# Optimization experiments

Measured on AMD Instinct MI355X. Metric: run time of the kernel, lower is better.

The kernel has to match this reference:

```python
import jax, jax.numpy as jnp
import numpy as np

N_NODES = 100000
N_EDGES = 3200000
N_FEAT = 128
EMB = 64


def setup_inputs() -> dict:
    key = jax.random.key(0)
    ks = jax.random.split(key, 10)
    x = jax.random.normal(ks[0], (N_NODES, N_FEAT), dtype=jnp.float32)
    edge_index = jax.random.randint(ks[1], (2, N_EDGES), 0, N_NODES, dtype=jnp.int64)
    batch_index = jnp.zeros((N_NODES,), dtype=jnp.int64)
    def glorot(k, fan_in, fan_out):
        s = jnp.sqrt(2.0 / (fan_in + fan_out)).astype(jnp.float32)
        return jax.random.normal(k, (fan_in, fan_out), dtype=jnp.float32) * s
    return {
        "x": x,
        "edge_index": edge_index,
        "batch_index": batch_index,
        "W0": glorot(ks[2], N_FEAT, EMB), "b0": jnp.zeros((EMB,), jnp.float32),
        "W1": glorot(ks[3], EMB, EMB),    "b1": jnp.zeros((EMB,), jnp.float32),
        "W2": glorot(ks[4], EMB, EMB),    "b2": jnp.zeros((EMB,), jnp.float32),
        "W3": glorot(ks[5], EMB, EMB),    "b3": jnp.zeros((EMB,), jnp.float32),
        "Wout": glorot(ks[6], EMB, 1),    "bout": jnp.zeros((1,), jnp.float32),
    }


def _gcn_norm(edge_index, n_nodes):
    # Add self-loops, compute symmetric normalization D^{-1/2} A_hat D^{-1/2}.
    loops = jnp.arange(n_nodes, dtype=edge_index.dtype)
    src = jnp.concatenate([edge_index[0], loops])  # message sources
    dst = jnp.concatenate([edge_index[1], loops])  # aggregation targets
    ones = jnp.ones(src.shape[0], dtype=jnp.float32)
    deg = jax.ops.segment_sum(ones, dst, num_segments=n_nodes)
    dinv = jnp.where(deg > 0, jax.lax.rsqrt(deg), 0.0)
    norm = dinv[src] * dinv[dst]  # [E + N]
    return src, dst, norm


def _gcn_conv(h, src, dst, norm, W, b, n_nodes):
    h = h @ W                              # [N, out]
    msg = h[src] * norm[:, None]           # gather + scale
    agg = jax.ops.segment_sum(msg, dst, num_segments=n_nodes)  # scatter-add
    return agg + b


def reference(x, edge_index, batch_index, W0, b0, W1, b1, W2, b2, W3, b3, Wout, bout):
    n = x.shape[0]
    src, dst, norm = _gcn_norm(edge_index, n)
    y = _gcn_conv(x, src, dst, norm, W0, b0, n)
    y = _gcn_conv(y, src, dst, norm, W1, b1, n)
    y = _gcn_conv(y, src, dst, norm, W2, b2, n)
    y = _gcn_conv(y, src, dst, norm, W3, b3, n)
    out = y @ Wout + bout
    return (out, y)
```

## Files before the change

kernel.cpp:

```cpp
#include <hip/hip_runtime.h>
#include <hip/hip_fp16.h>


#define FEAT 128
#define EMB 64
#define BINSHIFT 8
#define BINSIZE 256
#define NBIN 391
#define CHUNK 8192


__global__ __launch_bounds__(256) void bin_count_k(
    const int* __restrict__ dst, int* __restrict__ bincnt, int E) {
    __shared__ int hist[NBIN];
    int t = threadIdx.x;
    int base = blockIdx.x * CHUNK;
    int end = min(base + CHUNK, E);
    for (int i = t; i < NBIN; i += 256) hist[i] = 0;
    __syncthreads();
    for (int e = base + t; e < end; e += 256)
        atomicAdd(&hist[dst[e] >> BINSHIFT], 1);
    __syncthreads();
    for (int b = t; b < NBIN; b += 256) {
        int c = hist[b];
        if (c > 0) atomicAdd(&bincnt[b], c);
    }
}

__global__ void binscan_k(const int* __restrict__ bincnt, int* __restrict__ binptr,
                          int* __restrict__ bincur, int nbin, int E) {
    __shared__ int s[512];
    int t = threadIdx.x;
    int v = (t < nbin) ? bincnt[t] : 0;
    s[t] = v;
    __syncthreads();
    for (int off = 1; off < 512; off <<= 1) {
        int tv = (t >= off) ? s[t - off] : 0;
        __syncthreads();
        s[t] += tv;
        __syncthreads();
    }
    if (t < nbin) {
        int excl = s[t] - v;
        binptr[t] = excl;
        bincur[t] = excl;
    }
    if (t == 0) binptr[nbin] = E;
}

__global__ __launch_bounds__(256) void bin_edges_k(
    const int* __restrict__ src, const int* __restrict__ dst,
    int* __restrict__ bincur, int* __restrict__ ebuf, int E) {
    __shared__ int hist[NBIN];
    __shared__ int lcur[NBIN];
    int t = threadIdx.x;
    int base = blockIdx.x * CHUNK;
    int end = min(base + CHUNK, E);
    for (int i = t; i < NBIN; i += 256) hist[i] = 0;
    __syncthreads();
    for (int e = base + t; e < end; e += 256)
        atomicAdd(&hist[dst[e] >> BINSHIFT], 1);
    __syncthreads();
    for (int b = t; b < NBIN; b += 256) {
        int c = hist[b];
        lcur[b] = (c > 0) ? atomicAdd(&bincur[b], c) : 0;
    }
    __syncthreads();
    for (int e = base + t; e < end; e += 256) {
        int d = dst[e];
        int bin = d >> BINSHIFT;
        int r = atomicAdd(&lcur[bin], 1);
        ebuf[r] = src[e] | ((d & (BINSIZE - 1)) << 24);
    }
}

__global__ __launch_bounds__(256) void build_csr_k(
    const int* __restrict__ ebuf, const int* __restrict__ binptr,
    int* __restrict__ rowptr, float* __restrict__ dinv,
    int* __restrict__ col, int N, int E, int nbin) {
    __shared__ int lcnt[BINSIZE];
    __shared__ int lscan[BINSIZE];
    __shared__ int lcur[BINSIZE];
    int b = blockIdx.x;
    int t = threadIdx.x;
    int n0 = b << BINSHIFT;
    int e0 = binptr[b];
    int e1 = binptr[b + 1];

    lcnt[t] = 0;
    __syncthreads();
    for (int i = e0 + t; i < e1; i += 256)
        atomicAdd(&lcnt[((unsigned)ebuf[i]) >> 24], 1);
    __syncthreads();

    int v = lcnt[t];
    lscan[t] = v;
    __syncthreads();
    for (int off = 1; off < 256; off <<= 1) {
        int tv = (t >= off) ? lscan[t - off] : 0;
        __syncthreads();
        lscan[t] += tv;
        __syncthreads();
    }
    int excl = e0 + lscan[t] - v;
    lcur[t] = excl;
    if (n0 + t < N) {
        rowptr[n0 + t] = excl;
        dinv[n0 + t] = 1.0f / sqrtf((float)(v + 1));
    }
    if (b == nbin - 1 && t == 0) rowptr[N] = E;
    __syncthreads();

    for (int i = e0 + t; i < e1; i += 256) {
        int w = ebuf[i];
        int dl = ((unsigned)w) >> 24;
        int p = atomicAdd(&lcur[dl], 1);
        col[p] = (w & 0xFFFFFF) << 7;
    }
}


#define AKP 68

template <int K>
__global__ __launch_bounds__(256) void gemm_scale_k(
    const float* __restrict__ H, const float* __restrict__ W,
    const float* __restrict__ dinv, __half* __restrict__ G, int N) {
    __shared__ float Ws[K * EMB];
    __shared__ float As[64 * AKP];
    int t = threadIdx.x;
    int r0blk = blockIdx.x * 64;

    for (int i = t * 4; i < K * EMB; i += 1024)
        *(float4*)(Ws + i) = *(const float4*)(W + i);

    int tc = t & 15;
    int tr = t >> 4;
    int j0 = tc * 4;
    int r0 = r0blk + tr * 4;

    float acc[4][4] = {{0.f}};

    for (int k0 = 0; k0 < K; k0 += 64) {
#pragma unroll
        for (int n = 0; n < 4; n++) {
            int idx = t + n * 256;
            int row = idx >> 4;
            int cg  = idx & 15;
            int r = r0blk + row;
            if (r >= N) r = N - 1;
            *(float4*)(As + row * AKP + cg * 4) =
                *(const float4*)(H + (size_t)r * K + k0 + cg * 4);
        }
        __syncthreads();

#pragma unroll 2
        for (int k = 0; k < 64; k += 4) {
            float4 a[4];
#pragma unroll
            for (int i = 0; i < 4; i++)
                a[i] = *(const float4*)(As + (tr * 4 + i) * AKP + k);
#pragma unroll
            for (int kk = 0; kk < 4; kk++) {
                float4 wv = *(const float4*)(Ws + (k0 + k + kk) * EMB + j0);
#pragma unroll
                for (int i = 0; i < 4; i++) {
                    float av = (kk == 0) ? a[i].x : (kk == 1) ? a[i].y
                             : (kk == 2) ? a[i].z : a[i].w;
                    acc[i][0] = fmaf(av, wv.x, acc[i][0]);
                    acc[i][1] = fmaf(av, wv.y, acc[i][1]);
                    acc[i][2] = fmaf(av, wv.z, acc[i][2]);
                    acc[i][3] = fmaf(av, wv.w, acc[i][3]);
                }
            }
        }
        __syncthreads();
    }

#pragma unroll
    for (int i = 0; i < 4; i++) {
        if (r0 + i < N) {
            float s = dinv[r0 + i];
            union { __half2 h2[2]; float2 f2; } o;
            o.h2[0] = __floats2half2_rn(acc[i][0] * s, acc[i][1] * s);
            o.h2[1] = __floats2half2_rn(acc[i][2] * s, acc[i][3] * s);
            *(float2*)(G + (size_t)(r0 + i) * EMB + j0) = o.f2;
        }
    }
}


__device__ __forceinline__ void h8_acc(float (&a)[8], float4 raw) {
    union { float4 f4; __half2 h2[4]; } u;
    u.f4 = raw;
    float2 p0 = __half22float2(u.h2[0]);
    float2 p1 = __half22float2(u.h2[1]);
    float2 p2 = __half22float2(u.h2[2]);
    float2 p3 = __half22float2(u.h2[3]);
    a[0] += p0.x; a[1] += p0.y; a[2] += p1.x; a[3] += p1.y;
    a[4] += p2.x; a[5] += p2.y; a[6] += p3.x; a[7] += p3.y;
}

__device__ __forceinline__ void agg_node8(const __half* __restrict__ G,
                                          const int* __restrict__ coff,
                                          int s, int e, int selfoff,
                                          int grp, int f8, float (&r)[8]) {
    const char* Gb = (const char*)G + f8 * 16;
    float a0[8] = {0.f, 0.f, 0.f, 0.f, 0.f, 0.f, 0.f, 0.f};
    float a1[8] = {0.f, 0.f, 0.f, 0.f, 0.f, 0.f, 0.f, 0.f};
    float a2[8] = {0.f, 0.f, 0.f, 0.f, 0.f, 0.f, 0.f, 0.f};
    float a3[8] = {0.f, 0.f, 0.f, 0.f, 0.f, 0.f, 0.f, 0.f};
    if (grp == 0) h8_acc(a0, *(const float4*)(Gb + selfoff));

    int i = s;
    if (i + 32 <= e) {
        int c0 = coff[i + grp];
        int c1 = coff[i + 8 + grp];
        int c2 = coff[i + 16 + grp];
        int c3 = coff[i + 24 + grp];
        while (true) {
            float4 g0 = *(const float4*)(Gb + (size_t)(unsigned)c0);
            float4 g1 = *(const float4*)(Gb + (size_t)(unsigned)c1);
            float4 g2 = *(const float4*)(Gb + (size_t)(unsigned)c2);
            float4 g3 = *(const float4*)(Gb + (size_t)(unsigned)c3);
            i += 32;
            bool more = (i + 32 <= e);
            if (more) {
                c0 = coff[i + grp];
                c1 = coff[i + 8 + grp];
                c2 = coff[i + 16 + grp];
                c3 = coff[i + 24 + grp];
            }
            h8_acc(a0, g0);
            h8_acc(a1, g1);
            h8_acc(a2, g2);
            h8_acc(a3, g3);
            if (!more) break;
        }
    }
    for (; i + 8 <= e; i += 8) {
        float4 g = *(const float4*)(Gb + (size_t)(unsigned)coff[i + grp]);
        h8_acc(a1, g);
    }
    if (grp < e - i) {
        float4 g = *(const float4*)(Gb + (size_t)(unsigned)coff[i + grp]);
        h8_acc(a2, g);
    }

#pragma unroll
    for (int k = 0; k < 8; k++) {
        float v = (a0[k] + a1[k]) + (a2[k] + a3[k]);
        v += __shfl_xor(v, 8, 64);
        v += __shfl_xor(v, 16, 64);
        v += __shfl_xor(v, 32, 64);
        r[k] = v;
    }
}

__global__ __launch_bounds__(256) void agg_k(
    const __half* __restrict__ G, const float* __restrict__ dinv,
    const int* __restrict__ rowptr, const int* __restrict__ coff,
    const float* __restrict__ bias, float* __restrict__ Hout, int N) {
    int gw = (blockIdx.x * 256 + threadIdx.x) >> 6;
    int lane = threadIdx.x & 63;
    if (gw >= N) return;
    gw = __builtin_amdgcn_readfirstlane(gw);
    int grp = lane >> 3;
    int f8 = lane & 7;
    int s = rowptr[gw], e = rowptr[gw + 1];
    float r[8];
    agg_node8(G, coff, s, e, gw << 7, grp, f8, r);
    if (grp == 0) {
        float d = dinv[gw];
        float4 b0v = *(const float4*)(bias + f8 * 8);
        float4 b1v = *(const float4*)(bias + f8 * 8 + 4);
        float4 lo = make_float4(r[0] * d + b0v.x, r[1] * d + b0v.y,
                                r[2] * d + b0v.z, r[3] * d + b0v.w);
        float4 hi = make_float4(r[4] * d + b1v.x, r[5] * d + b1v.y,
                                r[6] * d + b1v.z, r[7] * d + b1v.w);
        float* o = Hout + (size_t)gw * EMB + f8 * 8;
        *(float4*)o = lo;
        *(float4*)(o + 4) = hi;
    }
}

__global__ __launch_bounds__(256) void agg_final_k(
    const __half* __restrict__ G, const float* __restrict__ dinv,
    const int* __restrict__ rowptr, const int* __restrict__ coff,
    const float* __restrict__ bias, const float* __restrict__ Wout,
    const float* __restrict__ bout, float* __restrict__ Y,
    float* __restrict__ Out, int N) {
    int gw = (blockIdx.x * 256 + threadIdx.x) >> 6;
    int lane = threadIdx.x & 63;
    if (gw >= N) return;
    gw = __builtin_amdgcn_readfirstlane(gw);
    int grp = lane >> 3;
    int f8 = lane & 7;
    int s = rowptr[gw], e = rowptr[gw + 1];
    float r[8];
    agg_node8(G, coff, s, e, gw << 7, grp, f8, r);
    float d = dinv[gw];
    float4 b0v = *(const float4*)(bias + f8 * 8);
    float4 b1v = *(const float4*)(bias + f8 * 8 + 4);
    float v0 = r[0] * d + b0v.x, v1 = r[1] * d + b0v.y;
    float v2 = r[2] * d + b0v.z, v3 = r[3] * d + b0v.w;
    float v4 = r[4] * d + b1v.x, v5 = r[5] * d + b1v.y;
    float v6 = r[6] * d + b1v.z, v7 = r[7] * d + b1v.w;
    if (grp == 0) {
        float* o = Y + (size_t)gw * EMB + f8 * 8;
        *(float4*)o = make_float4(v0, v1, v2, v3);
        *(float4*)(o + 4) = make_float4(v4, v5, v6, v7);
    }
    float4 w0v = *(const float4*)(Wout + f8 * 8);
    float4 w1v = *(const float4*)(Wout + f8 * 8 + 4);
    float p = v0 * w0v.x + v1 * w0v.y + v2 * w0v.z + v3 * w0v.w +
              v4 * w1v.x + v5 * w1v.y + v6 * w1v.z + v7 * w1v.w;
    p += __shfl_xor(p, 1, 8);
    p += __shfl_xor(p, 2, 8);
    p += __shfl_xor(p, 4, 8);
    if (lane == 0) Out[gw] = p + bout[0];
}


extern "C" void kernel_launch(void* const* d_in, const int* in_sizes, int n_in,
                              void* d_out, int out_size, void* d_ws, size_t ws_size,
                              hipStream_t stream) {
    const float* x    = (const float*)d_in[0];
    const int*   ei   = (const int*)d_in[1];
    const float* W0   = (const float*)d_in[3];
    const float* b0   = (const float*)d_in[4];
    const float* W1   = (const float*)d_in[5];
    const float* b1   = (const float*)d_in[6];
    const float* W2   = (const float*)d_in[7];
    const float* b2   = (const float*)d_in[8];
    const float* W3   = (const float*)d_in[9];
    const float* b3   = (const float*)d_in[10];
    const float* Wout = (const float*)d_in[11];
    const float* bout = (const float*)d_in[12];

    const int N = in_sizes[0] / FEAT;
    const int E = in_sizes[1] / 2;
    const int* srcp = ei;
    const int* dstp = ei + E;
    const int nbin = (N + BINSIZE - 1) / BINSIZE;

    const int NP = ((N + 64) + 63) / 64 * 64;
    float* dinv  = (float*)d_ws;
    int* rowptr  = (int*)(dinv + NP);
    int* bincnt  = rowptr + NP;
    int* binptr  = bincnt + 1024;
    int* bincur  = binptr + 1024;
    int* col     = bincur + 1024;
    float* bufA  = (float*)(col + ((E + 63) / 64) * 64);
    int* ebuf    = (int*)bufA;
    __half* Gbuf = (__half*)bufA;

    float* Out = (float*)d_out;
    float* Y   = Out + N;

    const int gemm_blocks = (N + 63) / 64;
    const int agg_blocks  = (N + 3) / 4;
    const int nchunk = (E + CHUNK - 1) / CHUNK;

    hipMemsetAsync(bincnt, 0, 1024 * sizeof(int), stream);
    bin_count_k<<<nchunk, 256, 0, stream>>>(dstp, bincnt, E);
    binscan_k<<<1, 512, 0, stream>>>(bincnt, binptr, bincur, nbin, E);
    bin_edges_k<<<nchunk, 256, 0, stream>>>(srcp, dstp, bincur, ebuf, E);
    build_csr_k<<<nbin, 256, 0, stream>>>(ebuf, binptr, rowptr, dinv, col, N, E, nbin);

    gemm_scale_k<FEAT><<<gemm_blocks, 256, 0, stream>>>(x, W0, dinv, Gbuf, N);
    agg_k<<<agg_blocks, 256, 0, stream>>>(Gbuf, dinv, rowptr, col, b0, Y, N);
    gemm_scale_k<EMB><<<gemm_blocks, 256, 0, stream>>>(Y, W1, dinv, Gbuf, N);
    agg_k<<<agg_blocks, 256, 0, stream>>>(Gbuf, dinv, rowptr, col, b1, Y, N);
    gemm_scale_k<EMB><<<gemm_blocks, 256, 0, stream>>>(Y, W2, dinv, Gbuf, N);
    agg_k<<<agg_blocks, 256, 0, stream>>>(Gbuf, dinv, rowptr, col, b2, Y, N);
    gemm_scale_k<EMB><<<gemm_blocks, 256, 0, stream>>>(Y, W3, dinv, Gbuf, N);
    agg_final_k<<<agg_blocks, 256, 0, stream>>>(Gbuf, dinv, rowptr, col, b3, Wout, bout,
                                                Y, Out, N);
}
```

Before: 555.2 us.

## Fuse next-layer GEMM into aggregation kernel and make first GEMM persistent

```diff
diff --git a/kernel.cpp b/kernel.cpp
--- a/kernel.cpp
+++ b/kernel.cpp
@@ -123,13 +123,12 @@
 #define AKP 68
 
 template <int K>
-__global__ __launch_bounds__(256) void gemm_scale_k(
+__global__ __launch_bounds__(256, 4) void gemm_scale_k(
     const float* __restrict__ H, const float* __restrict__ W,
-    const float* __restrict__ dinv, __half* __restrict__ G, int N) {
+    const float* __restrict__ dinv, __half* __restrict__ G, int N, int ntile) {
     __shared__ float Ws[K * EMB];
     __shared__ float As[64 * AKP];
     int t = threadIdx.x;
-    int r0blk = blockIdx.x * 64;
 
     for (int i = t * 4; i < K * EMB; i += 1024)
         *(float4*)(Ws + i) = *(const float4*)(W + i);
@@ -137,54 +136,57 @@
     int tc = t & 15;
     int tr = t >> 4;
     int j0 = tc * 4;
-    int r0 = r0blk + tr * 4;
-
-    float acc[4][4] = {{0.f}};
-
-    for (int k0 = 0; k0 < K; k0 += 64) {
-#pragma unroll
-        for (int n = 0; n < 4; n++) {
-            int idx = t + n * 256;
-            int row = idx >> 4;
-            int cg  = idx & 15;
-            int r = r0blk + row;
-            if (r >= N) r = N - 1;
-            *(float4*)(As + row * AKP + cg * 4) =
-                *(const float4*)(H + (size_t)r * K + k0 + cg * 4);
-        }
-        __syncthreads();
+
+    for (int tile = blockIdx.x; tile < ntile; tile += gridDim.x) {
+        int r0blk = tile * 64;
+        float acc[4][4] = {{0.f}};
+
+        for (int k0 = 0; k0 < K; k0 += 64) {
+            __syncthreads();
+#pragma unroll
+            for (int n = 0; n < 4; n++) {
+                int idx = t + n * 256;
+                int row = idx >> 4;
+                int cg  = idx & 15;
+                int r = r0blk + row;
+                if (r >= N) r = N - 1;
+                *(float4*)(As + row * AKP + cg * 4) =
+                    *(const float4*)(H + (size_t)r * K + k0 + cg * 4);
+            }
+            __syncthreads();
 
 #pragma unroll 2
-        for (int k = 0; k < 64; k += 4) {
-            float4 a[4];
-#pragma unroll
-            for (int i = 0; i < 4; i++)
-                a[i] = *(const float4*)(As + (tr * 4 + i) * AKP + k);
-#pragma unroll
-            for (int kk = 0; kk < 4; kk++) {
-                float4 wv = *(const float4*)(Ws + (k0 + k + kk) * EMB + j0);
-#pragma unroll
-                for (int i = 0; i < 4; i++) {
-                    float av = (kk == 0) ? a[i].x : (kk == 1) ? a[i].y
-                             : (kk == 2) ? a[i].z : a[i].w;
-                    acc[i][0] = fmaf(av, wv.x, acc[i][0]);
-                    acc[i][1] = fmaf(av, wv.y, acc[i][1]);
-                    acc[i][2] = fmaf(av, wv.z, acc[i][2]);
-                    acc[i][3] = fmaf(av, wv.w, acc[i][3]);
+            for (int k = 0; k < 64; k += 4) {
+                float4 a[4];
+#pragma unroll
+                for (int i = 0; i < 4; i++)
+                    a[i] = *(const float4*)(As + (tr * 4 + i) * AKP + k);
+#pragma unroll
+                for (int kk = 0; kk < 4; kk++) {
+                    float4 wv = *(const float4*)(Ws + (k0 + k + kk) * EMB + j0);
+#pragma unroll
+                    for (int i = 0; i < 4; i++) {
+                        float av = (kk == 0) ? a[i].x : (kk == 1) ? a[i].y
+                                 : (kk == 2) ? a[i].z : a[i].w;
+                        acc[i][0] = fmaf(av, wv.x, acc[i][0]);
+                        acc[i][1] = fmaf(av, wv.y, acc[i][1]);
+                        acc[i][2] = fmaf(av, wv.z, acc[i][2]);
+                        acc[i][3] = fmaf(av, wv.w, acc[i][3]);
+                    }
                 }
             }
         }
-        __syncthreads();
-    }
-
-#pragma unroll
-    for (int i = 0; i < 4; i++) {
-        if (r0 + i < N) {
-            float s = dinv[r0 + i];
-            union { __half2 h2[2]; float2 f2; } o;
-            o.h2[0] = __floats2half2_rn(acc[i][0] * s, acc[i][1] * s);
-            o.h2[1] = __floats2half2_rn(acc[i][2] * s, acc[i][3] * s);
-            *(float2*)(G + (size_t)(r0 + i) * EMB + j0) = o.f2;
+
+        int r0 = r0blk + tr * 4;
+#pragma unroll
+        for (int i = 0; i < 4; i++) {
+            if (r0 + i < N) {
+                float s = dinv[r0 + i];
+                union { __half2 h2[2]; float2 f2; } o;
+                o.h2[0] = __floats2half2_rn(acc[i][0] * s, acc[i][1] * s);
+                o.h2[1] = __floats2half2_rn(acc[i][2] * s, acc[i][3] * s);
+                *(float2*)(G + (size_t)(r0 + i) * EMB + j0) = o.f2;
+            }
         }
     }
 }
@@ -257,12 +259,24 @@
     }
 }
 
-__global__ __launch_bounds__(256) void agg_k(
+
+#define WNP 68
+
+__global__ __launch_bounds__(256) void agg_gemm_k(
     const __half* __restrict__ G, const float* __restrict__ dinv,
     const int* __restrict__ rowptr, const int* __restrict__ coff,
-    const float* __restrict__ bias, float* __restrict__ Hout, int N) {
-    int gw = (blockIdx.x * 256 + threadIdx.x) >> 6;
-    int lane = threadIdx.x & 63;
+    const float* __restrict__ bias, const float* __restrict__ Wn,
+    __half* __restrict__ Gout, int N) {
+    __shared__ float Wls[EMB * WNP];
+    int t = threadIdx.x;
+    for (int i = t * 4; i < EMB * EMB; i += 1024) {
+        int k = i >> 6, o = i & 63;
+        *(float4*)(Wls + k * WNP + o) = *(const float4*)(Wn + i);
+    }
+    __syncthreads();
+
+    int gw = (blockIdx.x * 256 + t) >> 6;
+    int lane = t & 63;
     if (gw >= N) return;
     gw = __builtin_amdgcn_readfirstlane(gw);
     int grp = lane >> 3;
@@ -270,19 +284,43 @@
     int s = rowptr[gw], e = rowptr[gw + 1];
     float r[8];
     agg_node8(G, coff, s, e, gw << 7, grp, f8, r);
-    if (grp == 0) {
-        float d = dinv[gw];
-        float4 b0v = *(const float4*)(bias + f8 * 8);
-        float4 b1v = *(const float4*)(bias + f8 * 8 + 4);
-        float4 lo = make_float4(r[0] * d + b0v.x, r[1] * d + b0v.y,
-                                r[2] * d + b0v.z, r[3] * d + b0v.w);
-        float4 hi = make_float4(r[4] * d + b1v.x, r[5] * d + b1v.y,
-                                r[6] * d + b1v.z, r[7] * d + b1v.w);
-        float* o = Hout + (size_t)gw * EMB + f8 * 8;
-        *(float4*)o = lo;
-        *(float4*)(o + 4) = hi;
-    }
-}
+    float d = dinv[gw];
+    float4 b0v = *(const float4*)(bias + f8 * 8);
+    float4 b1v = *(const float4*)(bias + f8 * 8 + 4);
+    float h[8];
+    h[0] = r[0] * d + b0v.x; h[1] = r[1] * d + b0v.y;
+    h[2] = r[2] * d + b0v.z; h[3] = r[3] * d + b0v.w;
+    h[4] = r[4] * d + b1v.x; h[5] = r[5] * d + b1v.y;
+    h[6] = r[6] * d + b1v.z; h[7] = r[7] * d + b1v.w;
+
+    float p[8] = {0.f, 0.f, 0.f, 0.f, 0.f, 0.f, 0.f, 0.f};
+#pragma unroll
+    for (int rr = 0; rr < 8; rr++) {
+        const float* wrow = Wls + (f8 * 8 + rr) * WNP + grp * 8;
+        float4 wa = *(const float4*)(wrow);
+        float4 wb = *(const float4*)(wrow + 4);
+        float hv = h[rr];
+        p[0] = fmaf(hv, wa.x, p[0]); p[1] = fmaf(hv, wa.y, p[1]);
+        p[2] = fmaf(hv, wa.z, p[2]); p[3] = fmaf(hv, wa.w, p[3]);
+        p[4] = fmaf(hv, wb.x, p[4]); p[5] = fmaf(hv, wb.y, p[5]);
+        p[6] = fmaf(hv, wb.z, p[6]); p[7] = fmaf(hv, wb.w, p[7]);
+    }
+#pragma unroll
+    for (int k = 0; k < 8; k++) {
+        p[k] += __shfl_xor(p[k], 1, 64);
+        p[k] += __shfl_xor(p[k], 2, 64);
+        p[k] += __shfl_xor(p[k], 4, 64);
+    }
+    if (f8 == 0) {
+        union { __half2 h2[4]; float4 f4; } o;
+        o.h2[0] = __floats2half2_rn(p[0] * d, p[1] * d);
+        o.h2[1] = __floats2half2_rn(p[2] * d, p[3] * d);
+        o.h2[2] = __floats2half2_rn(p[4] * d, p[5] * d);
+        o.h2[3] = __floats2half2_rn(p[6] * d, p[7] * d);
+        *(float4*)((char*)Gout + ((size_t)gw << 7) + grp * 16) = o.f4;
+    }
+}
+
 
 __global__ __launch_bounds__(256) void agg_final_k(
     const __half* __restrict__ G, const float* __restrict__ dinv,
@@ -353,13 +391,15 @@
     int* col     = bincur + 1024;
     float* bufA  = (float*)(col + ((E + 63) / 64) * 64);
     int* ebuf    = (int*)bufA;
-    __half* Gbuf = (__half*)bufA;
+    __half* Gbuf0 = (__half*)bufA;
+    __half* Gbuf1 = Gbuf0 + (size_t)N * EMB;
 
     float* Out = (float*)d_out;
     float* Y   = Out + N;
 
-    const int gemm_blocks = (N + 63) / 64;
-    const int agg_blocks  = (N + 3) / 4;
+    const int ntile = (N + 63) / 64;
+    const int gemm_grid = (ntile < 768) ? ntile : 768;
+    const int agg_blocks = (N + 3) / 4;
     const int nchunk = (E + CHUNK - 1) / CHUNK;
 
     hipMemsetAsync(bincnt, 0, 1024 * sizeof(int), stream);
@@ -368,13 +408,10 @@
     bin_edges_k<<<nchunk, 256, 0, stream>>>(srcp, dstp, bincur, ebuf, E);
     build_csr_k<<<nbin, 256, 0, stream>>>(ebuf, binptr, rowptr, dinv, col, N, E, nbin);
 
-    gemm_scale_k<FEAT><<<gemm_blocks, 256, 0, stream>>>(x, W0, dinv, Gbuf, N);
-    agg_k<<<agg_blocks, 256, 0, stream>>>(Gbuf, dinv, rowptr, col, b0, Y, N);
-    gemm_scale_k<EMB><<<gemm_blocks, 256, 0, stream>>>(Y, W1, dinv, Gbuf, N);
-    agg_k<<<agg_blocks, 256, 0, stream>>>(Gbuf, dinv, rowptr, col, b1, Y, N);
-    gemm_scale_k<EMB><<<gemm_blocks, 256, 0, stream>>>(Y, W2, dinv, Gbuf, N);
-    agg_k<<<agg_blocks, 256, 0, stream>>>(Gbuf, dinv, rowptr, col, b2, Y, N);
-    gemm_scale_k<EMB><<<gemm_blocks, 256, 0, stream>>>(Y, W3, dinv, Gbuf, N);
-    agg_final_k<<<agg_blocks, 256, 0, stream>>>(Gbuf, dinv, rowptr, col, b3, Wout, bout,
+    gemm_scale_k<FEAT><<<gemm_grid, 256, 0, stream>>>(x, W0, dinv, Gbuf0, N, ntile);
+    agg_gemm_k<<<agg_blocks, 256, 0, stream>>>(Gbuf0, dinv, rowptr, col, b0, W1, Gbuf1, N);
+    agg_gemm_k<<<agg_blocks, 256, 0, stream>>>(Gbuf1, dinv, rowptr, col, b1, W2, Gbuf0, N);
+    agg_gemm_k<<<agg_blocks, 256, 0, stream>>>(Gbuf0, dinv, rowptr, col, b2, W3, Gbuf1, N);
+    agg_final_k<<<agg_blocks, 256, 0, stream>>>(Gbuf1, dinv, rowptr, col, b3, Wout, bout,
                                                 Y, Out, N);
 }
```

New measurement: 608.9 us. 1.1x slower.

## Store intermediate layer activations in fp16 and make GEMM grid persistent

Applied to the files above, without the earlier changes.

```diff
diff --git a/kernel.cpp b/kernel.cpp
--- a/kernel.cpp
+++ b/kernel.cpp
@@ -123,13 +123,12 @@
 #define AKP 68
 
 template <int K>
-__global__ __launch_bounds__(256) void gemm_scale_k(
+__global__ __launch_bounds__(256, 4) void gemm_scale_k(
     const float* __restrict__ H, const float* __restrict__ W,
-    const float* __restrict__ dinv, __half* __restrict__ G, int N) {
+    const float* __restrict__ dinv, __half* __restrict__ G, int N, int ntile) {
     __shared__ float Ws[K * EMB];
     __shared__ float As[64 * AKP];
     int t = threadIdx.x;
-    int r0blk = blockIdx.x * 64;
 
     for (int i = t * 4; i < K * EMB; i += 1024)
         *(float4*)(Ws + i) = *(const float4*)(W + i);
@@ -137,20 +136,97 @@
     int tc = t & 15;
     int tr = t >> 4;
     int j0 = tc * 4;
-    int r0 = r0blk + tr * 4;
-
-    float acc[4][4] = {{0.f}};
-
-    for (int k0 = 0; k0 < K; k0 += 64) {
-#pragma unroll
-        for (int n = 0; n < 4; n++) {
+
+    for (int tile = blockIdx.x; tile < ntile; tile += gridDim.x) {
+        int r0blk = tile * 64;
+        float acc[4][4] = {{0.f}};
+
+        for (int k0 = 0; k0 < K; k0 += 64) {
+            __syncthreads();
+#pragma unroll
+            for (int n = 0; n < 4; n++) {
+                int idx = t + n * 256;
+                int row = idx >> 4;
+                int cg  = idx & 15;
+                int r = r0blk + row;
+                if (r >= N) r = N - 1;
+                *(float4*)(As + row * AKP + cg * 4) =
+                    *(const float4*)(H + (size_t)r * K + k0 + cg * 4);
+            }
+            __syncthreads();
+
+#pragma unroll 2
+            for (int k = 0; k < 64; k += 4) {
+                float4 a[4];
+#pragma unroll
+                for (int i = 0; i < 4; i++)
+                    a[i] = *(const float4*)(As + (tr * 4 + i) * AKP + k);
+#pragma unroll
+                for (int kk = 0; kk < 4; kk++) {
+                    float4 wv = *(const float4*)(Ws + (k0 + k + kk) * EMB + j0);
+#pragma unroll
+                    for (int i = 0; i < 4; i++) {
+                        float av = (kk == 0) ? a[i].x : (kk == 1) ? a[i].y
+                                 : (kk == 2) ? a[i].z : a[i].w;
+                        acc[i][0] = fmaf(av, wv.x, acc[i][0]);
+                        acc[i][1] = fmaf(av, wv.y, acc[i][1]);
+                        acc[i][2] = fmaf(av, wv.z, acc[i][2]);
+                        acc[i][3] = fmaf(av, wv.w, acc[i][3]);
+                    }
+                }
+            }
+        }
+
+        int r0 = r0blk + tr * 4;
+#pragma unroll
+        for (int i = 0; i < 4; i++) {
+            if (r0 + i < N) {
+                float s = dinv[r0 + i];
+                union { __half2 h2[2]; float2 f2; } o;
+                o.h2[0] = __floats2half2_rn(acc[i][0] * s, acc[i][1] * s);
+                o.h2[1] = __floats2half2_rn(acc[i][2] * s, acc[i][3] * s);
+                *(float2*)(G + (size_t)(r0 + i) * EMB + j0) = o.f2;
+            }
+        }
+    }
+}
+
+
+__global__ __launch_bounds__(256, 4) void gemm_scale_h_k(
+    const __half* __restrict__ Hh, const float* __restrict__ W,
+    const float* __restrict__ dinv, __half* __restrict__ G, int N, int ntile) {
+    __shared__ float Ws[EMB * EMB];
+    __shared__ float As[64 * AKP];
+    int t = threadIdx.x;
+
+    for (int i = t * 4; i < EMB * EMB; i += 1024)
+        *(float4*)(Ws + i) = *(const float4*)(W + i);
+
+    int tc = t & 15;
+    int tr = t >> 4;
+    int j0 = tc * 4;
+
+    for (int tile = blockIdx.x; tile < ntile; tile += gridDim.x) {
+        int r0blk = tile * 64;
+        float acc[4][4] = {{0.f}};
+
+        __syncthreads();
+#pragma unroll
+        for (int n = 0; n < 2; n++) {
             int idx = t + n * 256;
-            int row = idx >> 4;
-            int cg  = idx & 15;
+            int row = idx >> 3;
+            int hg  = idx & 7;
             int r = r0blk + row;
             if (r >= N) r = N - 1;
-            *(float4*)(As + row * AKP + cg * 4) =
-                *(const float4*)(H + (size_t)r * K + k0 + cg * 4);
+            union { float4 f4; __half2 h2[4]; } u;
+            u.f4 = *(const float4*)(Hh + (size_t)r * EMB + hg * 8);
+            float* dst = As + row * AKP + hg * 8;
+            float2 p0 = __half22float2(u.h2[0]);
+            float2 p1 = __half22float2(u.h2[1]);
+            float2 p2 = __half22float2(u.h2[2]);
+            float2 p3 = __half22float2(u.h2[3]);
+            dst[0] = p0.x; dst[1] = p0.y; dst[2] = p1.x; dst[3] = p1.y;
+            dst[4] = p2.x; dst[5] = p2.y; dst[6] = p3.x; dst[7] = p3.y;
         }
         __syncthreads();
 
@@ -162,7 +238,7 @@
                 a[i] = *(const float4*)(As + (tr * 4 + i) * AKP + k);
 #pragma unroll
             for (int kk = 0; kk < 4; kk++) {
-                float4 wv = *(const float4*)(Ws + (k0 + k + kk) * EMB + j0);
+                float4 wv = *(const float4*)(Ws + (k + kk) * EMB + j0);
 #pragma unroll
                 for (int i = 0; i < 4; i++) {
                     float av = (kk == 0) ? a[i].x : (kk == 1) ? a[i].y
@@ -174,17 +250,17 @@
                 }
             }
         }
-        __syncthreads();
-    }
-
-#pragma unroll
-    for (int i = 0; i < 4; i++) {
-        if (r0 + i < N) {
-            float s = dinv[r0 + i];
-            union { __half2 h2[2]; float2 f2; } o;
-            o.h2[0] = __floats2half2_rn(acc[i][0] * s, acc[i][1] * s);
-            o.h2[1] = __floats2half2_rn(acc[i][2] * s, acc[i][3] * s);
-            *(float2*)(G + (size_t)(r0 + i) * EMB + j0) = o.f2;
+
+        int r0 = r0blk + tr * 4;
+#pragma unroll
+        for (int i = 0; i < 4; i++) {
+            if (r0 + i < N) {
+                float s = dinv[r0 + i];
+                union { __half2 h2[2]; float2 f2; } o;
+                o.h2[0] = __floats2half2_rn(acc[i][0] * s, acc[i][1] * s);
+                o.h2[1] = __floats2half2_rn(acc[i][2] * s, acc[i][3] * s);
+                *(float2*)(G + (size_t)(r0 + i) * EMB + j0) = o.f2;
+            }
         }
     }
 }
@@ -257,10 +333,10 @@
     }
 }
 
-__global__ __launch_bounds__(256) void agg_k(
+__global__ __launch_bounds__(256) void agg_h_k(
     const __half* __restrict__ G, const float* __restrict__ dinv,
     const int* __restrict__ rowptr, const int* __restrict__ coff,
-    const float* __restrict__ bias, float* __restrict__ Hout, int N) {
+    const float* __restrict__ bias, __half* __restrict__ Hout, int N) {
     int gw = (blockIdx.x * 256 + threadIdx.x) >> 6;
     int lane = threadIdx.x & 63;
     if (gw >= N) return;
@@ -274,13 +350,12 @@
         float d = dinv[gw];
         float4 b0v = *(const float4*)(bias + f8 * 8);
         float4 b1v = *(const float4*)(bias + f8 * 8 + 4);
-        float4 lo = make_float4(r[0] * d + b0v.x, r[1] * d + b0v.y,
-                                r[2] * d + b0v.z, r[3] * d + b0v.w);
-        float4 hi = make_float4(r[4] * d + b1v.x, r[5] * d + b1v.y,
-                                r[6] * d + b1v.z, r[7] * d + b1v.w);
-        float* o = Hout + (size_t)gw * EMB + f8 * 8;
-        *(float4*)o = lo;
-        *(float4*)(o + 4) = hi;
+        union { __half2 h2[4]; float4 f4; } o;
+        o.h2[0] = __floats2half2_rn(r[0] * d + b0v.x, r[1] * d + b0v.y);
+        o.h2[1] = __floats2half2_rn(r[2] * d + b0v.z, r[3] * d + b0v.w);
+        o.h2[2] = __floats2half2_rn(r[4] * d + b1v.x, r[5] * d + b1v.y);
+        o.h2[3] = __floats2half2_rn(r[6] * d + b1v.z, r[7] * d + b1v.w);
+        *(float4*)((char*)Hout + ((size_t)gw << 7) + f8 * 16) = o.f4;
     }
 }
 
@@ -354,12 +429,14 @@
     float* bufA  = (float*)(col + ((E + 63) / 64) * 64);
     int* ebuf    = (int*)bufA;
     __half* Gbuf = (__half*)bufA;
+    __half* Yh   = Gbuf + (size_t)N * EMB;
 
     float* Out = (float*)d_out;
     float* Y   = Out + N;
 
-    const int gemm_blocks = (N + 63) / 64;
-    const int agg_blocks  = (N + 3) / 4;
+    const int ntile = (N + 63) / 64;
+    const int gemm_grid = (ntile < 768) ? ntile : 768;
+    const int agg_blocks = (N + 3) / 4;
     const int nchunk = (E + CHUNK - 1) / CHUNK;
 
     hipMemsetAsync(bincnt, 0, 1024 * sizeof(int), stream);
@@ -368,13 +445,13 @@
     bin_edges_k<<<nchunk, 256, 0, stream>>>(srcp, dstp, bincur, ebuf, E);
     build_csr_k<<<nbin, 256, 0, stream>>>(ebuf, binptr, rowptr, dinv, col, N, E, nbin);
 
-    gemm_scale_k<FEAT><<<gemm_blocks, 256, 0, stream>>>(x, W0, dinv, Gbuf, N);
-    agg_k<<<agg_blocks, 256, 0, stream>>>(Gbuf, dinv, rowptr, col, b0, Y, N);
-    gemm_scale_k<EMB><<<gemm_blocks, 256, 0, stream>>>(Y, W1, dinv, Gbuf, N);
-    agg_k<<<agg_blocks, 256, 0, stream>>>(Gbuf, dinv, rowptr, col, b1, Y, N);
-    gemm_scale_k<EMB><<<gemm_blocks, 256, 0, stream>>>(Y, W2, dinv, Gbuf, N);
-    agg_k<<<agg_blocks, 256, 0, stream>>>(Gbuf, dinv, rowptr, col, b2, Y, N);
-    gemm_scale_k<EMB><<<gemm_blocks, 256, 0, stream>>>(Y, W3, dinv, Gbuf, N);
+    gemm_scale_k<FEAT><<<gemm_grid, 256, 0, stream>>>(x, W0, dinv, Gbuf, N, ntile);
+    agg_h_k<<<agg_blocks, 256, 0, stream>>>(Gbuf, dinv, rowptr, col, b0, Yh, N);
+    gemm_scale_h_k<<<gemm_grid, 256, 0, stream>>>(Yh, W1, dinv, Gbuf, N, ntile);
+    agg_h_k<<<agg_blocks, 256, 0, stream>>>(Gbuf, dinv, rowptr, col, b1, Yh, N);
+    gemm_scale_h_k<<<gemm_grid, 256, 0, stream>>>(Yh, W2, dinv, Gbuf, N, ntile);
+    agg_h_k<<<agg_blocks, 256, 0, stream>>>(Gbuf, dinv, rowptr, col, b2, Yh, N);
+    gemm_scale_h_k<<<gemm_grid, 256, 0, stream>>>(Yh, W3, dinv, Gbuf, N, ntile);
     agg_final_k<<<agg_blocks, 256, 0, stream>>>(Gbuf, dinv, rowptr, col, b3, Wout, bout,
                                                 Y, Out, N);
 }
```

New measurement: 579.2 us. +4.3%, slower.

## Fold linear GCN layers into one combined weight and propagate biases via scalar vectors

Applied to the files above, without the earlier changes.

```diff
diff --git a/kernel.cpp b/kernel.cpp
--- a/kernel.cpp
+++ b/kernel.cpp
@@ -120,16 +120,72 @@
 }
 
 
+__global__ __launch_bounds__(256) void smallmats_k(
+    const float* __restrict__ W0, const float* __restrict__ W1,
+    const float* __restrict__ W2, const float* __restrict__ W3,
+    const float* __restrict__ b0, const float* __restrict__ b1,
+    const float* __restrict__ b2,
+    float* __restrict__ Wc, float* __restrict__ cbuf) {
+    __shared__ float T1[64 * 65];
+    __shared__ float T2[64 * 65];
+    int t = threadIdx.x;
+    for (int idx = t; idx < 4096; idx += 256) {
+        int i = idx >> 6, j = idx & 63;
+        float s = 0.f;
+        for (int k = 0; k < 64; k++) s = fmaf(W2[i * 64 + k], W3[k * 64 + j], s);
+        T1[i * 65 + j] = s;
+    }
+    __syncthreads();
+    for (int idx = t; idx < 4096; idx += 256) {
+        int i = idx >> 6, j = idx & 63;
+        float s = 0.f;
+        for (int k = 0; k < 64; k++) s = fmaf(W1[i * 64 + k], T1[k * 65 + j], s);
+        T2[i * 65 + j] = s;
+    }
+    __syncthreads();
+    for (int idx = t; idx < 8192; idx += 256) {
+        int i = idx >> 6, j = idx & 63;
+        float s = 0.f;
+        for (int k = 0; k < 64; k++) s = fmaf(W0[i * 64 + k], T2[k * 65 + j], s);
+        Wc[idx] = s;
+    }
+    if (t < 64) {
+        float s0 = 0.f, s1 = 0.f, s2 = 0.f;
+        for (int k = 0; k < 64; k++) {
+            s0 = fmaf(b0[k], T2[k * 65 + t], s0);
+            s1 = fmaf(b1[k], T1[k * 65 + t], s1);
+            s2 = fmaf(b2[k], W3[k * 64 + t], s2);
+        }
+        cbuf[t] = s0; cbuf[64 + t] = s1; cbuf[128 + t] = s2;
+    }
+}
+
+
+__global__ __launch_bounds__(256) void svec_k(
+    const float* __restrict__ w, const float* __restrict__ dinv,
+    const int* __restrict__ rowptr, const int* __restrict__ coff,
+    float* __restrict__ u, float* __restrict__ wnext, int N) {
+    int i = blockIdx.x * 256 + threadIdx.x;
+    if (i >= N) return;
+    int s = rowptr[i], e = rowptr[i + 1];
+    float acc = w[i];
+    for (int j = s; j < e; j++)
+        acc += w[((unsigned)coff[j]) >> 7];
+    float d = dinv[i];
+    u[i] = d * acc;
+    wnext[i] = d * d * acc;
+}
+
+
 #define AKP 68
 
 template <int K>
-__global__ __launch_bounds__(256) void gemm_scale_k(
+__global__ __launch_bounds__(256, 4) void gemm_scale_k(
     const float* __restrict__ H, const float* __restrict__ W,
-    const float* __restrict__ dinv, __half* __restrict__ G, int N) {
+    const float* __restrict__ dinv, __half* __restrict__ G, int N, int ntile) {
     __shared__ float Ws[K * EMB];
     __shared__ float As[64 * AKP];
     int t = threadIdx.x;
-    int r0blk = blockIdx.x * 64;
 
     for (int i = t * 4; i < K * EMB; i += 1024)
         *(float4*)(Ws + i) = *(const float4*)(W + i);
@@ -137,54 +193,57 @@
     int tc = t & 15;
     int tr = t >> 4;
     int j0 = tc * 4;
-    int r0 = r0blk + tr * 4;
-
-    float acc[4][4] = {{0.f}};
-
-    for (int k0 = 0; k0 < K; k0 += 64) {
-#pragma unroll
-        for (int n = 0; n < 4; n++) {
-            int idx = t + n * 256;
-            int row = idx >> 4;
-            int cg  = idx & 15;
-            int r = r0blk + row;
-            if (r >= N) r = N - 1;
-            *(float4*)(As + row * AKP + cg * 4) =
-                *(const float4*)(H + (size_t)r * K + k0 + cg * 4);
-        }
-        __syncthreads();
+
+    for (int tile = blockIdx.x; tile < ntile; tile += gridDim.x) {
+        int r0blk = tile * 64;
+        float acc[4][4] = {{0.f}};
+
+        for (int k0 = 0; k0 < K; k0 += 64) {
+            __syncthreads();
+#pragma unroll
+            for (int n = 0; n < 4; n++) {
+                int idx = t + n * 256;
+                int row = idx >> 4;
+                int cg  = idx & 15;
+                int r = r0blk + row;
+                if (r >= N) r = N - 1;
+                *(float4*)(As + row * AKP + cg * 4) =
+                    *(const float4*)(H + (size_t)r * K + k0 + cg * 4);
+            }
+            __syncthreads();
 
 #pragma unroll 2
-        for (int k = 0; k < 64; k += 4) {
-            float4 a[4];
-#pragma unroll
-            for (int i = 0; i < 4; i++)
-                a[i] = *(const float4*)(As + (tr * 4 + i) * AKP + k);
-#pragma unroll
-            for (int kk = 0; kk < 4; kk++) {
-                float4 wv = *(const float4*)(Ws + (k0 + k + kk) * EMB + j0);
-#pragma unroll
-                for (int i = 0; i < 4; i++) {
-                    float av = (kk == 0) ? a[i].x : (kk == 1) ? a[i].y
-                             : (kk == 2) ? a[i].z : a[i].w;
-                    acc[i][0] = fmaf(av, wv.x, acc[i][0]);
-                    acc[i][1] = fmaf(av, wv.y, acc[i][1]);
-                    acc[i][2] = fmaf(av, wv.z, acc[i][2]);
-                    acc[i][3] = fmaf(av, wv.w, acc[i][3]);
+            for (int k = 0; k < 64; k += 4) {
+                float4 a[4];
+#pragma unroll
+                for (int i = 0; i < 4; i++)
+                    a[i] = *(const float4*)(As + (tr * 4 + i) * AKP + k);
+#pragma unroll
+                for (int kk = 0; kk < 4; kk++) {
+                    float4 wv = *(const float4*)(Ws + (k0 + k + kk) * EMB + j0);
+#pragma unroll
+                    for (int i = 0; i < 4; i++) {
+                        float av = (kk == 0) ? a[i].x : (kk == 1) ? a[i].y
+                                 : (kk == 2) ? a[i].z : a[i].w;
+                        acc[i][0] = fmaf(av, wv.x, acc[i][0]);
+                        acc[i][1] = fmaf(av, wv.y, acc[i][1]);
+                        acc[i][2] = fmaf(av, wv.z, acc[i][2]);
+                        acc[i][3] = fmaf(av, wv.w, acc[i][3]);
+                    }
                 }
             }
         }
-        __syncthreads();
-    }
-
-#pragma unroll
-    for (int i = 0; i < 4; i++) {
-        if (r0 + i < N) {
-            float s = dinv[r0 + i];
-            union { __half2 h2[2]; float2 f2; } o;
-            o.h2[0] = __floats2half2_rn(acc[i][0] * s, acc[i][1] * s);
-            o.h2[1] = __floats2half2_rn(acc[i][2] * s, acc[i][3] * s);
-            *(float2*)(G + (size_t)(r0 + i) * EMB + j0) = o.f2;
+
+        int r0 = r0blk + tr * 4;
+#pragma unroll
+        for (int i = 0; i < 4; i++) {
+            if (r0 + i < N) {
+                float s = dinv[r0 + i];
+                union { __half2 h2[2]; float2 f2; } o;
+                o.h2[0] = __floats2half2_rn(acc[i][0] * s, acc[i][1] * s);
+                o.h2[1] = __floats2half2_rn(acc[i][2] * s, acc[i][3] * s);
+                *(float2*)(G + (size_t)(r0 + i) * EMB + j0) = o.f2;
+            }
         }
     }
 }
@@ -257,10 +316,10 @@
     }
 }
 
-__global__ __launch_bounds__(256) void agg_k(
+__global__ __launch_bounds__(256) void agg_mid_k(
     const __half* __restrict__ G, const float* __restrict__ dinv,
     const int* __restrict__ rowptr, const int* __restrict__ coff,
-    const float* __restrict__ bias, float* __restrict__ Hout, int N) {
+    __half* __restrict__ Gout, int N) {
     int gw = (blockIdx.x * 256 + threadIdx.x) >> 6;
     int lane = threadIdx.x & 63;
     if (gw >= N) return;
@@ -272,22 +331,22 @@
     agg_node8(G, coff, s, e, gw << 7, grp, f8, r);
     if (grp == 0) {
         float d = dinv[gw];
-        float4 b0v = *(const float4*)(bias + f8 * 8);
-        float4 b1v = *(const float4*)(bias + f8 * 8 + 4);
-        float4 lo = make_float4(r[0] * d + b0v.x, r[1] * d + b0v.y,
-                                r[2] * d + b0v.z, r[3] * d + b0v.w);
-        float4 hi = make_float4(r[4] * d + b1v.x, r[5] * d + b1v.y,
-                                r[6] * d + b1v.z, r[7] * d + b1v.w);
-        float* o = Hout + (size_t)gw * EMB + f8 * 8;
-        *(float4*)o = lo;
-        *(float4*)(o + 4) = hi;
+        float dd = d * d;
+        union { __half2 h2[4]; float4 f4; } o;
+        o.h2[0] = __floats2half2_rn(r[0] * dd, r[1] * dd);
+        o.h2[1] = __floats2half2_rn(r[2] * dd, r[3] * dd);
+        o.h2[2] = __floats2half2_rn(r[4] * dd, r[5] * dd);
+        o.h2[3] = __floats2half2_rn(r[6] * dd, r[7] * dd);
+        *(float4*)((char*)Gout + ((size_t)gw << 7) + f8 * 16) = o.f4;
     }
 }
 
 __global__ __launch_bounds__(256) void agg_final_k(
     const __half* __restrict__ G, const float* __restrict__ dinv,
     const int* __restrict__ rowptr, const int* __restrict__ coff,
-    const float* __restrict__ bias, const float* __restrict__ Wout,
+    const float* __restrict__ u0, const float* __restrict__ u1,
+    const float* __restrict__ u2, const float* __restrict__ cbuf,
+    const float* __restrict__ b3, const float* __restrict__ Wout,
     const float* __restrict__ bout, float* __restrict__ Y,
     float* __restrict__ Out, int N) {
     int gw = (blockIdx.x * 256 + threadIdx.x) >> 6;
@@ -300,21 +359,32 @@
     float r[8];
     agg_node8(G, coff, s, e, gw << 7, grp, f8, r);
     float d = dinv[gw];
-    float4 b0v = *(const float4*)(bias + f8 * 8);
-    float4 b1v = *(const float4*)(bias + f8 * 8 + 4);
-    float v0 = r[0] * d + b0v.x, v1 = r[1] * d + b0v.y;
-    float v2 = r[2] * d + b0v.z, v3 = r[3] * d + b0v.w;
-    float v4 = r[4] * d + b1v.x, v5 = r[5] * d + b1v.y;
-    float v6 = r[6] * d + b1v.z, v7 = r[7] * d + b1v.w;
+    float u0v = u0[gw], u1v = u1[gw], u2v = u2[gw];
+    const float* c0 = cbuf;
+    const float* c1 = cbuf + 64;
+    const float* c2 = cbuf + 128;
+    float v[8];
+#pragma unroll
+    for (int half = 0; half < 2; half++) {
+        int o4 = f8 * 8 + half * 4;
+        float4 c0v = *(const float4*)(c0 + o4);
+        float4 c1v = *(const float4*)(c1 + o4);
+        float4 c2v = *(const float4*)(c2 + o4);
+        float4 b3v = *(const float4*)(b3 + o4);
+        v[half * 4 + 0] = r[half * 4 + 0] * d + u2v * c0v.x + u1v * c1v.x + u0v * c2v.x + b3v.x;
+        v[half * 4 + 1] = r[half * 4 + 1] * d + u2v * c0v.y + u1v * c1v.y + u0v * c2v.y + b3v.y;
+        v[half * 4 + 2] = r[half * 4 + 2] * d + u2v * c0v.z + u1v * c1v.z + u0v * c2v.z + b3v.z;
+        v[half * 4 + 3] = r[half * 4 + 3] * d + u2v * c0v.w + u1v * c1v.w + u0v * c2v.w + b3v.w;
+    }
     if (grp == 0) {
         float* o = Y + (size_t)gw * EMB + f8 * 8;
-        *(float4*)o = make_float4(v0, v1, v2, v3);
-        *(float4*)(o + 4) = make_float4(v4, v5, v6, v7);
+        *(float4*)o = make_float4(v[0], v[1], v[2], v[3]);
+        *(float4*)(o + 4) = make_float4(v[4], v[5], v[6], v[7]);
     }
     float4 w0v = *(const float4*)(Wout + f8 * 8);
     float4 w1v = *(const float4*)(Wout + f8 * 8 + 4);
-    float p = v0 * w0v.x + v1 * w0v.y + v2 * w0v.z + v3 * w0v.w +
-              v4 * w1v.x + v5 * w1v.y + v6 * w1v.z + v7 * w1v.w;
+    float p = v[0] * w0v.x + v[1] * w0v.y + v[2] * w0v.z + v[3] * w0v.w +
+              v[4] * w1v.x + v[5] * w1v.y + v[6] * w1v.z + v[7] * w1v.w;
     p += __shfl_xor(p, 1, 8);
     p += __shfl_xor(p, 2, 8);
     p += __shfl_xor(p, 4, 8);
@@ -351,15 +421,25 @@
     int* binptr  = bincnt + 1024;
     int* bincur  = binptr + 1024;
     int* col     = bincur + 1024;
-    float* bufA  = (float*)(col + ((E + 63) / 64) * 64);
-    int* ebuf    = (int*)bufA;
-    __half* Gbuf = (__half*)bufA;
+    float* u0    = (float*)(col + ((E + 63) / 64) * 64);
+    float* u1    = u0 + NP;
+    float* u2    = u1 + NP;
+    float* Wc    = u2 + NP;
+    float* cbuf  = Wc + 8192;
+    float* gbase = cbuf + 256;
+    int* ebuf    = (int*)gbase;
+    __half* Gbuf0 = (__half*)gbase;
+    __half* Gbuf1 = Gbuf0 + (size_t)N * EMB;
+    float* wa    = (float*)(Gbuf1 + (size_t)N * EMB);
+    float* wb    = wa + NP;
 
     float* Out = (float*)d_out;
     float* Y   = Out + N;
 
-    const int gemm_blocks = (N + 63) / 64;
-    const int agg_blocks  = (N + 3) / 4;
+    const int ntile = (N + 63) / 64;
+    const int gemm_grid = (ntile < 768) ? ntile : 768;
+    const int agg_blocks = (N + 3) / 4;
+    const int svec_blocks = (N + 255) / 256;
     const int nchunk = (E + CHUNK - 1) / CHUNK;
 
     hipMemsetAsync(bincnt, 0, 1024 * sizeof(int), stream);
@@ -368,13 +448,16 @@
     bin_edges_k<<<nchunk, 256, 0, stream>>>(srcp, dstp, bincur, ebuf, E);
     build_csr_k<<<nbin, 256, 0, stream>>>(ebuf, binptr, rowptr, dinv, col, N, E, nbin);
 
-    gemm_scale_k<FEAT><<<gemm_blocks, 256, 0, stream>>>(x, W0, dinv, Gbuf, N);
-    agg_k<<<agg_blocks, 256, 0, stream>>>(Gbuf, dinv, rowptr, col, b0, Y, N);
-    gemm_scale_k<EMB><<<gemm_blocks, 256, 0, stream>>>(Y, W1, dinv, Gbuf, N);
-    agg_k<<<agg_blocks, 256, 0, stream>>>(Gbuf, dinv, rowptr, col, b1, Y, N);
-    gemm_scale_k<EMB><<<gemm_blocks, 256, 0, stream>>>(Y, W2, dinv, Gbuf, N);
-    agg_k<<<agg_blocks, 256, 0, stream>>>(Gbuf, dinv, rowptr, col, b2, Y, N);
-    gemm_scale_k<EMB><<<gemm_blocks, 256, 0, stream>>>(Y, W3, dinv, Gbuf, N);
-    agg_final_k<<<agg_blocks, 256, 0, stream>>>(Gbuf, dinv, rowptr, col, b3, Wout, bout,
+    smallmats_k<<<1, 256, 0, stream>>>(W0, W1, W2, W3, b0, b1, b2, Wc, cbuf);
+    svec_k<<<svec_blocks, 256, 0, stream>>>(dinv, dinv, rowptr, col, u0, wa, N);
+    svec_k<<<svec_blocks, 256, 0, stream>>>(wa, dinv, rowptr, col, u1, wb, N);
+    svec_k<<<svec_blocks, 256, 0, stream>>>(wb, dinv, rowptr, col, u2, wa, N);
+
+    gemm_scale_k<FEAT><<<gemm_grid, 256, 0, stream>>>(x, Wc, dinv, Gbuf0, N, ntile);
+    agg_mid_k<<<agg_blocks, 256, 0, stream>>>(Gbuf0, dinv, rowptr, col, Gbuf1, N);
+    agg_mid_k<<<agg_blocks, 256, 0, stream>>>(Gbuf1, dinv, rowptr, col, Gbuf0, N);
+    agg_mid_k<<<agg_blocks, 256, 0, stream>>>(Gbuf0, dinv, rowptr, col, Gbuf1, N);
+    agg_final_k<<<agg_blocks, 256, 0, stream>>>(Gbuf1, dinv, rowptr, col,
+                                                u0, u1, u2, cbuf, b3, Wout, bout,
                                                 Y, Out, N);
 }
```

Result: slower. 644.8 us (+16.1%).
